# Performance work log

Hardware: AMD Instinct MI355X
Metric: run time of the kernel (lower is better)

The kernel has to match this reference:

```python
import jax, jax.numpy as jnp
import numpy as np

D_MODEL, D_STATE, BATCH, SEQ = 512, 32, 8, 4096

def _hippo(n):
    i = np.arange(n)[:, None].astype(np.float64)
    j = np.arange(n)[None, :].astype(np.float64)
    P = np.where(i > j, np.sqrt(2 * i + 1) * np.sqrt(2 * j + 1), 0.0)
    P = P + np.diag(np.arange(1, n + 1).astype(np.float64))
    return (-P).astype(np.float32)

def setup_inputs() -> dict:
    key = jax.random.key(0)
    k0, k1, k2, k3 = jax.random.split(key, 4)
    x = jax.random.normal(k0, (BATCH, SEQ, D_MODEL), dtype=jnp.float32)
    A = jnp.asarray(_hippo(D_STATE))
    B = jax.random.normal(k1, (D_STATE, D_MODEL), dtype=jnp.float32) / np.float32(np.sqrt(D_MODEL))
    C = jax.random.normal(k2, (D_MODEL, D_STATE), dtype=jnp.float32) / np.float32(np.sqrt(D_STATE))
    D = jnp.ones((D_MODEL,), dtype=jnp.float32)
    log_dt = jnp.zeros((D_MODEL,), dtype=jnp.float32)
    W_out = jax.random.normal(k3, (D_MODEL, D_MODEL), dtype=jnp.float32) / np.float32(np.sqrt(D_MODEL))
    b_out = jnp.zeros((D_MODEL,), dtype=jnp.float32)
    return {"x": x, "A": A, "B": B, "C": C, "D": D, "log_dt": log_dt, "W_out": W_out, "b_out": b_out}

def reference(x, A, B, C, D, log_dt, W_out, b_out):
    # x: (b, s, d). S4 layer with bilinear discretization and tanh recurrence.
    n = A.shape[0]
    dt = jnp.mean(jnp.clip(jnp.exp(log_dt), 1e-4, 1.0))  # scalar dt.mean()
    I = jnp.eye(n, dtype=x.dtype)
    inv_term = jnp.linalg.inv(I - 0.5 * dt * A)
    A_bar = (I + 0.5 * dt * A) @ inv_term          # (n, n)
    B_bar = dt * (inv_term @ B)                    # (n, d)
    # Precompute input projection for all timesteps (vectorized):
    uB = jnp.einsum('bsd,nd->bsn', x, B_bar)       # (b, s, n)
    s0 = jnp.zeros((x.shape[0], n), dtype=x.dtype)
    def step(state, ub_t):
        state = jnp.tanh(state @ A_bar.T + ub_t)   # (b, n)
        return state, state
    final_state, states = jax.lax.scan(step, s0, jnp.swapaxes(uB, 0, 1))
    states = jnp.swapaxes(states, 0, 1)            # (b, s, n)
    y = jnp.einsum('bsn,dn->bsd', states, C) + x * D
    y = y @ W_out.T + b_out                        # output_proj (dropout = eval identity)
    return y, final_state
```

## Files before the change

### kernel.cpp

```cpp
#include <hip/hip_runtime.h>
#include <hip/hip_bf16.h>

#define D_MODEL 512
#define D_STATE 32
#define BATCH 8
#define SEQ 4096
#define MROWS (BATCH * SEQ)
#define NBLK 1024

typedef __bf16 bf16;
typedef __bf16 bf16x4 __attribute__((ext_vector_type(4)));
typedef __bf16 bf16x8 __attribute__((ext_vector_type(8)));
typedef float f32x4 __attribute__((ext_vector_type(4)));

#define CHUNK 16
#define BURN 80
#define NCHUNK (SEQ / CHUNK)

__global__ __launch_bounds__(256, 4) void k_A(
    const float* __restrict__ x, const float* __restrict__ A, const float* __restrict__ B,
    const float* __restrict__ C, const float* __restrict__ Dv, const float* __restrict__ log_dt,
    const float* __restrict__ W,
    float* __restrict__ A_bar, bf16* __restrict__ CW, bf16* __restrict__ WD,
    float* __restrict__ uB, bf16* __restrict__ xb) {
  __shared__ bf16 xt[32][512];
  __shared__ bf16 bfrag[2][1024];
  __shared__ float Xs[32][32];
  const int bid = blockIdx.x, t = threadIdx.x;
  const int w = t >> 6, lane = t & 63;
  const int l15 = lane & 15, kg = lane >> 4;
  float* Xf = &Xs[0][0];
  const long rowbase = (long)bid * 32;

  {
    float v0 = __expf(log_dt[t]);
    float v1 = __expf(log_dt[t + 256]);
    v0 = fminf(fmaxf(v0, 1e-4f), 1.0f);
    v1 = fminf(fmaxf(v1, 1e-4f), 1.0f);
    Xf[t] = v0 + v1;
  }
  {
    const int r = t >> 3, c0 = (t & 7) * 4;
    const float* xp = x + (rowbase + r) * D_MODEL + c0;
    bf16* xo = xb + (rowbase + r) * D_MODEL + c0;
    char* xrow = (char*)&xt[r][0];
    const int gb = (t & 7) >> 1;
    const int off8 = (t & 1) * 8;
    const int key = r & 7;
#pragma unroll
    for (int kt = 0; kt < 16; kt++) {
      const f32x4 v = *(const f32x4*)(xp + kt * 32);
      bf16x4 h;
      h[0] = (bf16)v[0]; h[1] = (bf16)v[1]; h[2] = (bf16)v[2]; h[3] = (bf16)v[3];
      *(bf16x4*)(xo + kt * 32) = h;
      *(bf16x4*)(xrow + (((kt * 4 + gb) ^ key) << 4) + off8) = h;
    }
  }
  __syncthreads();
  for (int s2 = 128; s2 > 0; s2 >>= 1) {
    if (t < s2) Xf[t] += Xf[t + s2];
    __syncthreads();
  }
  const float dtv = Xf[0] * (1.0f / 512.0f);
  __syncthreads();
  {
    const int i0 = 4 * t;
    const f32x4 av = *(const f32x4*)(A + i0);
    f32x4 mv;
#pragma unroll
    for (int q = 0; q < 4; q++) {
      const int r = (i0 + q) >> 5, c = (i0 + q) & 31;
      mv[q] = (r == c ? 1.0f : 0.0f) - 0.5f * dtv * av[q];
    }
    *(f32x4*)(Xf + i0) = mv;
  }
  __syncthreads();
  if (t < 32) {
    const int j = t;
    float xcol[32];
#pragma unroll
    for (int i = 0; i < 32; i++) {
      float s0 = 0.f, s1 = 0.f, s2 = 0.f, s3 = 0.f;
#pragma unroll
      for (int k = 0; k < 32; k += 4) {
        if (k < i)     s0 -= Xf[i * 32 + k]     * xcol[k];
        if (k + 1 < i) s1 -= Xf[i * 32 + k + 1] * xcol[k + 1];
        if (k + 2 < i) s2 -= Xf[i * 32 + k + 2] * xcol[k + 2];
        if (k + 3 < i) s3 -= Xf[i * 32 + k + 3] * xcol[k + 3];
      }
      const float num = (i == j ? 1.0f : 0.0f) + ((s0 + s1) + (s2 + s3));
      xcol[i] = (i >= j) ? num / Xf[i * 32 + i] : 0.0f;
    }
#pragma unroll
    for (int i = 0; i < 32; i++) Xs[i][j] = xcol[i];
  }
  __syncthreads();
  if (bid == 0) {
    const int i0 = 4 * t;
    const int r = t >> 3;
    f32x4 ov;
#pragma unroll
    for (int q = 0; q < 4; q++) {
      const int c = (i0 + q) & 31;
      float s = 0.f;
#pragma unroll
      for (int k = 0; k < 32; k++) {
        const float p2 = (r == k ? 1.0f : 0.0f) + 0.5f * dtv * A[r * 32 + k];
        s = fmaf(p2, Xf[k * 32 + c], s);
      }
      ov[q] = s;
    }
    *(f32x4*)(A_bar + i0) = ov;
  }
  const int m = w & 1, nf = w >> 1;
  f32x4 acc = (f32x4)(0.0f);
  {
    const int bn = t >> 3, bc0 = (t & 7) * 4;
    const int fbase = (((t & 7) >> 1) * 32 + bn) * 8 + (bc0 & 7);
    const int rdoff = (kg * 32 + nf * 16 + l15) * 8;
    const int arow = m * 16 + l15;
    const char* xrow = (const char*)&xt[arow][0];
    const int akey = l15 & 7;
#pragma unroll 1
    for (int kt = 0; kt < 16; kt++) {
      const f32x4 bv = *(const f32x4*)(B + bn * D_MODEL + kt * 32 + bc0);
      bf16x4 bh4, bl4;
#pragma unroll
      for (int q = 0; q < 4; q++) {
        const bf16 hi = (bf16)bv[q];
        bh4[q] = hi;
        bl4[q] = (bf16)(bv[q] - (float)hi);
      }
      *(bf16x4*)&bfrag[0][fbase] = bh4;
      *(bf16x4*)&bfrag[1][fbase] = bl4;
      __syncthreads();
      const bf16x8 af = *(const bf16x8*)(xrow + (((kt * 4 + kg) ^ akey) << 4));
      const bf16x8 bh = *(const bf16x8*)&bfrag[0][rdoff];
      const bf16x8 bl = *(const bf16x8*)&bfrag[1][rdoff];
      acc = __builtin_amdgcn_mfma_f32_16x16x32_bf16(af, bh, acc, 0, 0, 0);
      acc = __builtin_amdgcn_mfma_f32_16x16x32_bf16(af, bl, acc, 0, 0, 0);
      __syncthreads();
    }
  }
  float* srw = (float*)&xt[0][0];
  {
    const int col = nf * 16 + l15;
#pragma unroll
    for (int jj = 0; jj < 4; jj++)
      srw[(m * 16 + kg * 4 + jj) * 33 + col] = acc[jj];
  }
  __syncthreads();
  {
    const int n = t & 31, r0 = t >> 5;
    float u0 = 0.f, u1 = 0.f, u2 = 0.f, u3 = 0.f;
#pragma unroll
    for (int k2 = 0; k2 < 32; k2++) {
      const int k = (k2 + n) & 31;
      const float xv = Xf[n * 32 + k];
      u0 = fmaf(xv, srw[(r0)      * 33 + k], u0);
      u1 = fmaf(xv, srw[(r0 + 8)  * 33 + k], u1);
      u2 = fmaf(xv, srw[(r0 + 16) * 33 + k], u2);
      u3 = fmaf(xv, srw[(r0 + 24) * 33 + k], u3);
    }
    float* up = uB + (rowbase + r0) * D_STATE + n;
    up[0]                = dtv * u0;
    up[8 * D_STATE]      = dtv * u1;
    up[16 * D_STATE]     = dtv * u2;
    up[24 * D_STATE]     = dtv * u3;
  }
  if (bid >= 1 && bid <= 64) {
    const int idx = (bid - 1) * 256 + t;
    const int e = idx >> 5, n = idx & 31;
    float s = 0.f;
    for (int d = 0; d < D_MODEL; d += 4) {
      const f32x4 wv = *(const f32x4*)(W + e * D_MODEL + d);
      s = fmaf(wv[0], C[(d + 0) * D_STATE + n], s);
      s = fmaf(wv[1], C[(d + 1) * D_STATE + n], s);
      s = fmaf(wv[2], C[(d + 2) * D_STATE + n], s);
      s = fmaf(wv[3], C[(d + 3) * D_STATE + n], s);
    }
    CW[idx] = (bf16)s;
  } else if (bid >= 65 && bid <= 80) {
#pragma unroll
    for (int jj = 0; jj < 16; jj++) {
      const int i = (bid - 65) * 16384 + jj * 1024 + t * 4;
      const f32x4 wv = *(const f32x4*)(W + i);
      const f32x4 dv = *(const f32x4*)(Dv + (i & 511));
      bf16x4 h;
#pragma unroll
      for (int q = 0; q < 4; q++) h[q] = (bf16)(wv[q] * dv[q]);
      *(bf16x4*)(WD + i) = h;
    }
  }
}

__global__ void k_scan(const float* __restrict__ uB, const float* __restrict__ A_bar,
                       bf16* __restrict__ Sb, float* __restrict__ fs) {
  __shared__ float sbuf[256];
  const int t = threadIdx.x;
  const int g = t >> 5, n = t & 31;
  const int chain = blockIdx.x * 8 + g;
  const int b = chain >> 8;
  const int ch = chain & 255;
  const int cs = ch * CHUNK;
  const int t0 = cs - BURN;
  const int ce = cs + CHUNK;

  float a[32];
#pragma unroll
  for (int k = 0; k < 32; k += 4) {
    const f32x4 v = *(const f32x4*)(A_bar + n * 32 + k);
    a[k] = v[0]; a[k + 1] = v[1]; a[k + 2] = v[2]; a[k + 3] = v[3];
  }
#pragma unroll
  for (int k = 0; k < 32; k++) asm volatile("" : "+v"(a[k]));

  const float* ub = uB + (long)b * SEQ * D_STATE + n;
  bf16* sp = Sb + ((long)b * SEQ + cs) * D_STATE + n;
  float* myslot = &sbuf[g * 32];

  float s = 0.f;
  float ubuf[8], unext[8];
#pragma unroll
  for (int i = 0; i < 8; i++) {
    const int tt = t0 + i;
    ubuf[i] = (tt >= 0) ? ub[(long)tt * D_STATE] : 0.f;
  }
  for (int tg = t0; tg < ce; tg += 8) {
    const int tn = tg + 8;
#pragma unroll
    for (int i = 0; i < 8; i++) {
      const int tt = tn + i;
      unext[i] = (tt >= 0 && tt < ce) ? ub[(long)tt * D_STATE] : 0.f;
    }
#pragma unroll
    for (int i = 0; i < 8; i++) {
      const int tt = tg + i;
      myslot[n] = s;
      const f32x4 s0 = *(const f32x4*)(myslot + 0);
      const f32x4 s1 = *(const f32x4*)(myslot + 4);
      const f32x4 s2 = *(const f32x4*)(myslot + 8);
      const f32x4 s3 = *(const f32x4*)(myslot + 12);
      const f32x4 s4 = *(const f32x4*)(myslot + 16);
      const f32x4 s5 = *(const f32x4*)(myslot + 20);
      const f32x4 s6 = *(const f32x4*)(myslot + 24);
      const f32x4 s7 = *(const f32x4*)(myslot + 28);
      float acc0 = ubuf[i], acc1 = 0.f, acc2 = 0.f, acc3 = 0.f;
#pragma unroll
      for (int q = 0; q < 4; q++) {
        acc0 = fmaf(a[0 + q],  s0[q], acc0);
        acc1 = fmaf(a[4 + q],  s1[q], acc1);
        acc2 = fmaf(a[8 + q],  s2[q], acc2);
        acc3 = fmaf(a[12 + q], s3[q], acc3);
        acc0 = fmaf(a[16 + q], s4[q], acc0);
        acc1 = fmaf(a[20 + q], s5[q], acc1);
        acc2 = fmaf(a[24 + q], s6[q], acc2);
        acc3 = fmaf(a[28 + q], s7[q], acc3);
      }
      const float z = (acc0 + acc1) + (acc2 + acc3);
      const float e = __expf(2.f * z);
      const float r = __builtin_amdgcn_rcpf(e + 1.f);
      s = fmaf(-2.f, r, 1.f);
      if (tt >= cs) sp[(long)(tt - cs) * D_STATE] = (bf16)s;
    }
#pragma unroll
    for (int i = 0; i < 8; i++) ubuf[i] = unext[i];
  }
  if (ch == NCHUNK - 1) fs[b * D_STATE + n] = s;
}

__device__ __forceinline__ void stage_tile(const void* gbase, long row0, long rowStrideB,
                                           int kByte, void* lds, int w, int lane) {
#pragma unroll
  for (int j = 0; j < 2; j++) {
    const int base_off = (w << 11) + (j << 10);
    const int boff = base_off + (lane << 4);
    const int r = boff >> 6;
    const int s = (boff >> 4) & 3;
    const int cb = ((s ^ (r & 3)) << 4);
    const char* src = (const char*)gbase + (row0 + r) * rowStrideB + kByte + cb;
    __builtin_amdgcn_global_load_lds(
        (const __attribute__((address_space(1))) void*)src,
        (__attribute__((address_space(3))) void*)((char*)lds + base_off), 16, 0, 0);
  }
}

__global__ __launch_bounds__(256) void k_out(const bf16* __restrict__ xb,
                                             const bf16* __restrict__ WD,
                                             const bf16* __restrict__ Sb,
                                             const bf16* __restrict__ CW,
                                             const float* __restrict__ bias,
                                             float* __restrict__ out) {
  __shared__ bf16 As[2][128 * 32];
  __shared__ bf16 Bs[2][128 * 32];
  const int tid = threadIdx.x;
  const int w = tid >> 6, lane = tid & 63;
  const int swz = (blockIdx.x & 7) * 128 + (blockIdx.x >> 3);
  const int bm = swz >> 2, bn = swz & 3;
  const long rowbase = (long)bm * 128;
  const long colbase = (long)bn * 128;
  const int wr = w >> 1, wc = w & 1;
  const int l15 = lane & 15, kg = lane >> 4;
  const int kgs = kg ^ (l15 & 3);

  f32x4 acc[4][4];
#pragma unroll
  for (int m = 0; m < 4; m++)
#pragma unroll
    for (int n = 0; n < 4; n++) acc[m][n] = (f32x4)(0.0f);

  const int aoff = (wr * 64 + l15) * 32 + kgs * 8;
  const int boff = (wc * 64 + l15) * 32 + kgs * 8;

  auto STAGE = [&](int ti, int b) {
    if (ti < 16) {
      stage_tile(xb, rowbase, 1024, ti * 64, &As[b][0], w, lane);
      stage_tile(WD, colbase, 1024, ti * 64, &Bs[b][0], w, lane);
    } else {
      stage_tile(Sb, rowbase, 64, 0, &As[b][0], w, lane);
      stage_tile(CW, colbase, 64, 0, &Bs[b][0], w, lane);
    }
  };

  STAGE(0, 0);
  __syncthreads();
#pragma unroll 1
  for (int kt = 0; kt < 17; kt++) {
    const int cur = kt & 1;
    if (kt < 16) STAGE(kt + 1, cur ^ 1);
    bf16x8 af[4], bfr[4];
#pragma unroll
    for (int m = 0; m < 4; m++) af[m] = *(const bf16x8*)&As[cur][aoff + m * 16 * 32];
#pragma unroll
    for (int n = 0; n < 4; n++) bfr[n] = *(const bf16x8*)&Bs[cur][boff + n * 16 * 32];
#pragma unroll
    for (int m = 0; m < 4; m++)
#pragma unroll
      for (int n = 0; n < 4; n++)
        acc[m][n] = __builtin_amdgcn_mfma_f32_16x16x32_bf16(af[m], bfr[n], acc[m][n], 0, 0, 0);
    __syncthreads();
  }
#pragma unroll
  for (int n = 0; n < 4; n++) {
    const int e = (int)colbase + wc * 64 + n * 16 + l15;
    const float bv = bias[e];
#pragma unroll
    for (int m = 0; m < 4; m++) {
      const long r0 = rowbase + wr * 64 + m * 16 + kg * 4;
      const f32x4 v = acc[m][n];
#pragma unroll
      for (int jj = 0; jj < 4; jj++) out[(r0 + jj) * (long)D_MODEL + e] = v[jj] + bv;
    }
  }
}

extern "C" void kernel_launch(void* const* d_in, const int* in_sizes, int n_in,
                              void* d_out, int out_size, void* d_ws, size_t ws_size,
                              hipStream_t stream) {
  const float* x      = (const float*)d_in[0];
  const float* A      = (const float*)d_in[1];
  const float* B      = (const float*)d_in[2];
  const float* C      = (const float*)d_in[3];
  const float* Dv     = (const float*)d_in[4];
  const float* log_dt = (const float*)d_in[5];
  const float* W      = (const float*)d_in[6];
  const float* b_out  = (const float*)d_in[7];
  float* out = (float*)d_out;
  float* fs  = out + (long)MROWS * D_MODEL;

  char* ws = (char*)d_ws;
  float* A_bar = (float*)(ws + 0);
  bf16*  CW    = (bf16*)(ws + (68L << 10));
  bf16*  WD    = (bf16*)(ws + (100L << 10));
  bf16*  Sb    = (bf16*)(ws + (612L << 10));
  float* uB    = (float*)(ws + (2660L << 10));
  bf16*  xb    = (bf16*)(ws + (6756L << 10));

  k_A<<<dim3(NBLK), dim3(256), 0, stream>>>(x, A, B, C, Dv, log_dt, W,
                                            A_bar, CW, WD, uB, xb);
  k_scan<<<dim3(256), dim3(256), 0, stream>>>(uB, A_bar, Sb, fs);
  k_out<<<dim3((MROWS / 128) * (D_MODEL / 128)), dim3(256), 0, stream>>>(xb, WD, Sb, CW, b_out, out);
}
```

Baseline: 93.54 us.

## Load MFMA operands directly from global memory, dropping LDS staging and barriers

The x·B projection in k_A now has each lane load its MFMA A and B fragments straight from global memory and convert them to bf16 in registers. This replaces the swizzled LDS tile of x and the per-k-step B fragment staging, which needed two block barriers per iteration. It removes 32 __syncthreads and cuts shared memory from about 40KB to about 8KB, which may raise occupancy. In exchange x rows are read by two waves, each lane re-splits its B fragment into hi/lo parts, and the global loads are strided per lane rather than fully coalesced.

```diff
diff --git a/kernel.cpp b/kernel.cpp
--- a/kernel.cpp
+++ b/kernel.cpp
@@ -17,15 +17,21 @@
 #define BURN 80
 #define NCHUNK (SEQ / CHUNK)
 
+__device__ __forceinline__ bf16x8 cvt8(const f32x4 a, const f32x4 b) {
+  bf16x8 h;
+  h[0] = (bf16)a[0]; h[1] = (bf16)a[1]; h[2] = (bf16)a[2]; h[3] = (bf16)a[3];
+  h[4] = (bf16)b[0]; h[5] = (bf16)b[1]; h[6] = (bf16)b[2]; h[7] = (bf16)b[3];
+  return h;
+}
+
 __global__ __launch_bounds__(256, 4) void k_A(
     const float* __restrict__ x, const float* __restrict__ A, const float* __restrict__ B,
     const float* __restrict__ C, const float* __restrict__ Dv, const float* __restrict__ log_dt,
     const float* __restrict__ W,
     float* __restrict__ A_bar, bf16* __restrict__ CW, bf16* __restrict__ WD,
     float* __restrict__ uB, bf16* __restrict__ xb) {
-  __shared__ bf16 xt[32][512];
-  __shared__ bf16 bfrag[2][1024];
   __shared__ float Xs[32][32];
+  __shared__ float srw[32 * 33];
   const int bid = blockIdx.x, t = threadIdx.x;
   const int w = t >> 6, lane = t & 63;
   const int l15 = lane & 15, kg = lane >> 4;
@@ -38,23 +44,6 @@
     v0 = fminf(fmaxf(v0, 1e-4f), 1.0f);
     v1 = fminf(fmaxf(v1, 1e-4f), 1.0f);
     Xf[t] = v0 + v1;
-  }
-  {
-    const int r = t >> 3, c0 = (t & 7) * 4;
-    const float* xp = x + (rowbase + r) * D_MODEL + c0;
-    bf16* xo = xb + (rowbase + r) * D_MODEL + c0;
-    char* xrow = (char*)&xt[r][0];
-    const int gb = (t & 7) >> 1;
-    const int off8 = (t & 1) * 8;
-    const int key = r & 7;
-#pragma unroll
-    for (int kt = 0; kt < 16; kt++) {
-      const f32x4 v = *(const f32x4*)(xp + kt * 32);
-      bf16x4 h;
-      h[0] = (bf16)v[0]; h[1] = (bf16)v[1]; h[2] = (bf16)v[2]; h[3] = (bf16)v[3];
-      *(bf16x4*)(xo + kt * 32) = h;
-      *(bf16x4*)(xrow + (((kt * 4 + gb) ^ key) << 4) + off8) = h;
-    }
   }
   __syncthreads();
   for (int s2 = 128; s2 > 0; s2 >>= 1) {
@@ -94,6 +83,34 @@
 #pragma unroll
     for (int i = 0; i < 32; i++) Xs[i][j] = xcol[i];
   }
+
+  const int m = w & 1, nf = w >> 1;
+  const int arow = m * 16 + l15;
+  const int brow = nf * 16 + l15;
+  f32x4 acc = (f32x4)(0.0f);
+  {
+    const float* xp = x + (rowbase + arow) * D_MODEL + kg * 8;
+    bf16* xo = xb + (rowbase + arow) * D_MODEL + kg * 8;
+    const float* bp = B + brow * D_MODEL + kg * 8;
+#pragma unroll
+    for (int kt = 0; kt < 16; kt++) {
+      const f32x4 xa = *(const f32x4*)(xp + kt * 32);
+      const f32x4 xc = *(const f32x4*)(xp + kt * 32 + 4);
+      const bf16x8 af = cvt8(xa, xc);
+      if (nf == 0) *(bf16x8*)(xo + kt * 32) = af;
+      const f32x4 b0 = *(const f32x4*)(bp + kt * 32);
+      const f32x4 b1 = *(const f32x4*)(bp + kt * 32 + 4);
+      const bf16x8 bh = cvt8(b0, b1);
+      bf16x8 bl;
+#pragma unroll
+      for (int q = 0; q < 4; q++) {
+        bl[q]     = (bf16)(b0[q] - (float)bh[q]);
+        bl[q + 4] = (bf16)(b1[q] - (float)bh[q + 4]);
+      }
+      acc = __builtin_amdgcn_mfma_f32_16x16x32_bf16(af, bh, acc, 0, 0, 0);
+      acc = __builtin_amdgcn_mfma_f32_16x16x32_bf16(af, bl, acc, 0, 0, 0);
+    }
+  }
   __syncthreads();
   if (bid == 0) {
     const int i0 = 4 * t;
@@ -112,37 +129,6 @@
     }
     *(f32x4*)(A_bar + i0) = ov;
   }
-  const int m = w & 1, nf = w >> 1;
-  f32x4 acc = (f32x4)(0.0f);
-  {
-    const int bn = t >> 3, bc0 = (t & 7) * 4;
-    const int fbase = (((t & 7) >> 1) * 32 + bn) * 8 + (bc0 & 7);
-    const int rdoff = (kg * 32 + nf * 16 + l15) * 8;
-    const int arow = m * 16 + l15;
-    const char* xrow = (const char*)&xt[arow][0];
-    const int akey = l15 & 7;
-#pragma unroll 1
-    for (int kt = 0; kt < 16; kt++) {
-      const f32x4 bv = *(const f32x4*)(B + bn * D_MODEL + kt * 32 + bc0);
-      bf16x4 bh4, bl4;
-#pragma unroll
-      for (int q = 0; q < 4; q++) {
-        const bf16 hi = (bf16)bv[q];
-        bh4[q] = hi;
-        bl4[q] = (bf16)(bv[q] - (float)hi);
-      }
-      *(bf16x4*)&bfrag[0][fbase] = bh4;
-      *(bf16x4*)&bfrag[1][fbase] = bl4;
-      __syncthreads();
-      const bf16x8 af = *(const bf16x8*)(xrow + (((kt * 4 + kg) ^ akey) << 4));
-      const bf16x8 bh = *(const bf16x8*)&bfrag[0][rdoff];
-      const bf16x8 bl = *(const bf16x8*)&bfrag[1][rdoff];
-      acc = __builtin_amdgcn_mfma_f32_16x16x32_bf16(af, bh, acc, 0, 0, 0);
-      acc = __builtin_amdgcn_mfma_f32_16x16x32_bf16(af, bl, acc, 0, 0, 0);
-      __syncthreads();
-    }
-  }
-  float* srw = (float*)&xt[0][0];
   {
     const int col = nf * 16 + l15;
 #pragma unroll
@@ -163,10 +149,10 @@
       u3 = fmaf(xv, srw[(r0 + 24) * 33 + k], u3);
     }
     float* up = uB + (rowbase + r0) * D_STATE + n;
-    up[0]                = dtv * u0;
-    up[8 * D_STATE]      = dtv * u1;
-    up[16 * D_STATE]     = dtv * u2;
-    up[24 * D_STATE]     = dtv * u3;
+    up[0]            = dtv * u0;
+    up[8 * D_STATE]  = dtv * u1;
+    up[16 * D_STATE] = dtv * u2;
+    up[24 * D_STATE] = dtv * u3;
   }
   if (bid >= 1 && bid <= 64) {
     const int idx = (bid - 1) * 256 + t;
```

Result: slower. 100.7 us (+7.7%).
